# Performance work log

Hardware: AMD Instinct MI355X
Metric: run time of the kernel (lower is better)

The kernel has to match this reference:

```python
import jax, jax.numpy as jnp
import numpy as np

BN_EPS = 1e-5


def setup_inputs() -> dict:
    key = jax.random.key(0)
    ks = jax.random.split(key, 4)
    B, N, D = 8, 8192, 256
    outD = 256
    s = 1.0 / np.sqrt(D)
    return {
        "feature": jax.random.normal(ks[0], (B, N, D), dtype=jnp.float32),
        "W_qk": jax.random.normal(ks[1], (2, D, D), dtype=jnp.float32) * s,
        "b_qk": jnp.zeros((2, D), dtype=jnp.float32),
        "W_v": jax.random.normal(ks[2], (D, outD), dtype=jnp.float32) * s,
        "b_v": jnp.zeros((outD,), dtype=jnp.float32),
        "gamma": jnp.ones((D,), dtype=jnp.float32),
        "beta": jnp.zeros((D,), dtype=jnp.float32),
    }


def reference(feature, W_qk, b_qk, W_v, b_v, gamma, beta):
    # QK: [B, 2, N, D]
    QK = jnp.einsum("bnd,kde->bkne", feature, W_qk) + b_qk[None, :, None, :]
    # value: [B, N, outD]
    value = jnp.einsum("bnd,de->bne", feature, W_v) + b_v
    query = QK[:, 0]  # [B, N, D]
    key = QK[:, 1]    # [B, N, D]
    # softmax over the sequence axis (dim=1), per (batch, channel)
    sm = jax.nn.softmax(key, axis=1)
    # lambda context: softmax^T @ value -> [B, D, outD]
    lam = jnp.einsum("bnd,bne->bde", sm, value)
    # BatchNorm1d(featureDim) in training mode: channel axis = D (axis 1),
    # stats over (batch, spatial) = axes (0, 2); biased variance as torch uses.
    mean = jnp.mean(lam, axis=(0, 2), keepdims=True)
    var = jnp.var(lam, axis=(0, 2), keepdims=True)
    bn = (lam - mean) * jax.lax.rsqrt(var + BN_EPS)
    bn = bn * gamma[None, :, None] + beta[None, :, None]
    # result: query @ BN -> [B, N, outD]
    return jnp.einsum("bnd,bde->bne", query, bn)
```

## Files before the change

kernel.cpp:

```cpp
#include <hip/hip_runtime.h>

typedef unsigned short u16;
typedef __bf16 bf16x8 __attribute__((ext_vector_type(8)));
typedef float f32x4 __attribute__((ext_vector_type(4)));

#define LOG2E 1.44269504088896f

__device__ inline u16 f2b(float f) {
    unsigned u = __float_as_uint(f);
    u += 0x7fff + ((u >> 16) & 1);
    return (u16)(u >> 16);
}
__device__ inline float b2f(u16 u) { return __uint_as_float(((unsigned)u) << 16); }
__device__ inline unsigned pk2(float a, float b) {
    return (unsigned)f2b(a) | ((unsigned)f2b(b) << 16);
}
__device__ inline uint4 pack8(float4 a, float4 b) {
    return uint4{pk2(a.x, a.y), pk2(a.z, a.w), pk2(b.x, b.y), pk2(b.z, b.w)};
}
__device__ inline f32x4 mfma_bf16(uint4 a, uint4 b, f32x4 c) {
    return __builtin_amdgcn_mfma_f32_16x16x32_bf16(
        __builtin_bit_cast(bf16x8, a), __builtin_bit_cast(bf16x8, b), c, 0, 0, 0);
}
__device__ inline void ld16(const u16* g, u16* l) {
    __builtin_amdgcn_global_load_lds(
        (const __attribute__((address_space(1))) unsigned int*)g,
        (__attribute__((address_space(3))) unsigned int*)l, 16, 0, 0);
}
__device__ inline uint4 expfrag(uint4 v, float nc) {
    float e[8];
#pragma unroll
    for (int i = 0; i < 4; ++i) {
        unsigned u = ((const unsigned*)&v)[i];
        e[2 * i] = exp2f(fmaf(b2f((u16)(u & 0xffff)), LOG2E, nc));
        e[2 * i + 1] = exp2f(fmaf(b2f((u16)(u >> 16)), LOG2E, nc));
    }
    uint4 r;
    asm("v_cvt_pk_bf16_f32 %0, %1, %2" : "=v"(r.x) : "v"(e[0]), "v"(e[1]));
    asm("v_cvt_pk_bf16_f32 %0, %1, %2" : "=v"(r.y) : "v"(e[2]), "v"(e[3]));
    asm("v_cvt_pk_bf16_f32 %0, %1, %2" : "=v"(r.z) : "v"(e[4]), "v"(e[5]));
    asm("v_cvt_pk_bf16_f32 %0, %1, %2" : "=v"(r.w) : "v"(e[6]), "v"(e[7]));
    return r;
}


__global__ __launch_bounds__(256) void prep_w(const float* __restrict__ Wqk,
                                              const float* __restrict__ Wv,
                                              u16* __restrict__ WkT,
                                              u16* __restrict__ WvT,
                                              u16* __restrict__ Wqb) {
    int idx = blockIdx.x * 256 + threadIdx.x;
    int which = idx >> 16;
    int i = (idx >> 8) & 255;
    int j = idx & 255;
    if (which == 0)
        WkT[i * 256 + j] = f2b(Wqk[65536 + j * 256 + i]);
    else if (which == 1)
        WvT[i * 256 + j] = f2b(Wv[j * 256 + i]);
    else
        Wqb[i * 256 + j] = f2b(Wqk[i * 256 + j]);
}

__global__ __launch_bounds__(256, 2) void gemm_kv(const float* __restrict__ A,
                                                  const u16* __restrict__ BtK,
                                                  const u16* __restrict__ BtV,
                                                  const float* __restrict__ biasK,
                                                  const float* __restrict__ biasV,
                                                  u16* __restrict__ KT,
                                                  u16* __restrict__ VT,
                                                  float* __restrict__ partial) {
    __shared__ __align__(16) u16 lds[36864];

    const int t = threadIdx.x;
    const int r0 = blockIdx.x * 64;
    const int w = t >> 6, lane = t & 63, l15 = lane & 15, q = lane >> 4;
    const int sq = ((lane & 3) ^ ((lane >> 3) & 3)) * 8;
    const int qs = (q ^ ((l15 >> 1) & 3)) * 8;
    const int awoff = (t >> 2) * 32 + sq;
    const int brr = t >> 2;

    f32x4 accK[4][4], accV[4][4];
#pragma unroll
    for (int rt = 0; rt < 4; ++rt)
#pragma unroll
        for (int ct = 0; ct < 4; ++ct) {
            accK[rt][ct] = f32x4{0.f, 0.f, 0.f, 0.f};
            accV[rt][ct] = f32x4{0.f, 0.f, 0.f, 0.f};
        }

    const float* Arow = A + (long)(r0 + brr) * 256 + (t & 3) * 8;
    float4 p0 = ((const float4*)Arow)[0], p1 = ((const float4*)Arow)[1];
    float4 c0_ = *(const float4*)(Arow + 32), c1_ = *(const float4*)(Arow + 36);
    float4 d0_ = *(const float4*)(Arow + 64), d1_ = *(const float4*)(Arow + 68);

    {
        u16* dK = lds + 4096 + w * 512;
#pragma unroll
        for (int j = 0; j < 4; ++j) {
            int br = j * 64 + brr;
            ld16(BtK + br * 256 + sq, dK + j * 2048);
            ld16(BtV + br * 256 + sq, dK + 8192 + j * 2048);
        }
    }
    *(uint4*)(lds + awoff) = pack8(p0, p1);
    __syncthreads();

#pragma unroll
    for (int t8 = 0; t8 < 8; ++t8) {
        const int cur = t8 & 1;
        if (t8 < 7) {
            const int k0 = (t8 + 1) * 32;
            u16* dK = lds + 4096 + (cur ^ 1) * 16384 + w * 512;
#pragma unroll
            for (int j = 0; j < 4; ++j) {
                int br = j * 64 + brr;
                ld16(BtK + br * 256 + k0 + sq, dK + j * 2048);
                ld16(BtV + br * 256 + k0 + sq, dK + 8192 + j * 2048);
            }
            *(uint4*)(lds + (cur ^ 1) * 2048 + awoff) = pack8(c0_, c1_);
            c0_ = d0_; c1_ = d1_;
            if (t8 < 5) {
                d0_ = *(const float4*)(Arow + (t8 + 3) * 32);
                d1_ = *(const float4*)(Arow + (t8 + 3) * 32 + 4);
            }
        }
        const u16* Asc = lds + cur * 2048;
        const u16* Bc = lds + 4096 + cur * 16384;
        uint4 af[4];
#pragma unroll
        for (int rt = 0; rt < 4; ++rt)
            af[rt] = *(const uint4*)(Asc + (rt * 16 + l15) * 32 + qs);
#pragma unroll
        for (int ct = 0; ct < 4; ++ct) {
            const int bo = (w * 64 + ct * 16 + l15) * 32 + qs;
            uint4 bK = *(const uint4*)(Bc + bo);
            uint4 bV = *(const uint4*)(Bc + 8192 + bo);
#pragma unroll
            for (int rt = 0; rt < 4; ++rt) {
                accK[rt][ct] = mfma_bf16(af[rt], bK, accK[rt][ct]);
                accV[rt][ct] = mfma_bf16(af[rt], bV, accV[rt][ct]);
            }
        }
        __syncthreads();
    }

    const int bb = r0 >> 13;
    const int nt0 = (r0 & 8191) >> 5;
    const int nch = nt0 >> 1;
    u16* Ct = lds;
#pragma unroll
    for (int pass = 0; pass < 2; ++pass) {
        const f32x4(*acc)[4] = pass ? accV : accK;
        const float* bias = pass ? biasV : biasK;
        u16* CT = pass ? VT : KT;
#pragma unroll
        for (int ct = 0; ct < 4; ++ct) {
            const int col = w * 64 + ct * 16 + l15;
            const float bv = bias[col];
            ushort4 pks[4];
#pragma unroll
            for (int rt = 0; rt < 4; ++rt) {
                ushort4 pk;
                pk.x = f2b(acc[rt][ct][0] + bv);
                pk.y = f2b(acc[rt][ct][1] + bv);
                pk.z = f2b(acc[rt][ct][2] + bv);
                pk.w = f2b(acc[rt][ct][3] + bv);
                pks[rt] = pk;
                *(ushort4*)&Ct[col * 72 + rt * 16 + q * 4] = pk;
            }
            if (pass == 0) {
                float zm = -1e30f;
#pragma unroll
                for (int rt = 0; rt < 4; ++rt)
                    zm = fmaxf(zm,
                               fmaxf(fmaxf(b2f(pks[rt].x), b2f(pks[rt].y)),
                                     fmaxf(b2f(pks[rt].z), b2f(pks[rt].w))));
                zm = fmaxf(zm, __shfl_xor(zm, 16, 64));
                zm = fmaxf(zm, __shfl_xor(zm, 32, 64));
                zm *= LOG2E;
                float zs = 0.f;
#pragma unroll
                for (int rt = 0; rt < 4; ++rt) {
                    zs += exp2f(fmaf(b2f(pks[rt].x), LOG2E, -zm));
                    zs += exp2f(fmaf(b2f(pks[rt].y), LOG2E, -zm));
                    zs += exp2f(fmaf(b2f(pks[rt].z), LOG2E, -zm));
                    zs += exp2f(fmaf(b2f(pks[rt].w), LOG2E, -zm));
                }
                zs += __shfl_xor(zs, 16, 64);
                zs += __shfl_xor(zs, 32, 64);
                if (q == 0) {
                    float* pp =
                        partial + (((long)(bb * 128 + nch)) * 256 + col) * 2;
                    pp[0] = zm;
                    pp[1] = zs;
                }
            }
        }
        __syncthreads();
        {
            const long tb = (((long)(bb * 256 + nt0)) * 256 + t) * 32;
#pragma unroll
            for (int j2 = 0; j2 < 2; ++j2)
#pragma unroll
                for (int g = 0; g < 4; ++g)
                    *(uint4*)(CT + tb + j2 * 8192 + g * 8) =
                        *(const uint4*)&Ct[t * 72 + j2 * 32 + g * 8];
        }
        __syncthreads();
    }
}

__global__ __launch_bounds__(256) void stats2(const float* __restrict__ partial,
                                              float* __restrict__ ctab) {
    const int b = blockIdx.x, d = threadIdx.x;
    float M = -1e30f;
    for (int i = 0; i < 128; ++i)
        M = fmaxf(M, partial[(((long)(b * 128 + i)) * 256 + d) * 2]);
    float S = 0.f;
    for (int i = 0; i < 128; ++i) {
        const float* pp = partial + (((long)(b * 128 + i)) * 256 + d) * 2;
        S += pp[1] * exp2f(pp[0] - M);
    }
    ctab[b * 256 + d] = M + log2f(S);
}

__global__ __launch_bounds__(256, 3) void gemm_out(const float* __restrict__ A,
                                                   const u16* __restrict__ WfoldT,
                                                   const float* __restrict__ outb,
                                                   float* __restrict__ C) {
    __shared__ __align__(16) u16 lds[20480];
    const int t = threadIdx.x;
    const int r0 = blockIdx.x * 64;
    const int bb = r0 >> 13;
    const int w = t >> 6, lane = t & 63, l15 = lane & 15, q = lane >> 4;
    const int sq = ((lane & 3) ^ ((lane >> 3) & 3)) * 8;
    const int qs = (q ^ ((l15 >> 1) & 3)) * 8;
    const int awoff = (t >> 2) * 32 + sq;
    const int brr = t >> 2;
    const u16* Bt = WfoldT + (long)bb * 65536;

    f32x4 acc[4][4];
#pragma unroll
    for (int rt = 0; rt < 4; ++rt)
#pragma unroll
        for (int ct = 0; ct < 4; ++ct) acc[rt][ct] = f32x4{0.f, 0.f, 0.f, 0.f};

    const float* Arow = A + (long)(r0 + brr) * 256 + (t & 3) * 8;
    float4 p0 = ((const float4*)Arow)[0], p1 = ((const float4*)Arow)[1];
    float4 c0_ = *(const float4*)(Arow + 32), c1_ = *(const float4*)(Arow + 36);
    float4 d0_ = *(const float4*)(Arow + 64), d1_ = *(const float4*)(Arow + 68);

    {
        u16* dB = lds + 4096 + w * 512;
#pragma unroll
        for (int j = 0; j < 4; ++j)
            ld16(Bt + (j * 64 + brr) * 256 + sq, dB + j * 2048);
    }
    *(uint4*)(lds + awoff) = pack8(p0, p1);
    __syncthreads();

#pragma unroll
    for (int t8 = 0; t8 < 8; ++t8) {
        const int cur = t8 & 1;
        if (t8 < 7) {
            const int k0 = (t8 + 1) * 32;
            u16* dB = lds + 4096 + (cur ^ 1) * 8192 + w * 512;
#pragma unroll
            for (int j = 0; j < 4; ++j)
                ld16(Bt + (j * 64 + brr) * 256 + k0 + sq, dB + j * 2048);
            *(uint4*)(lds + (cur ^ 1) * 2048 + awoff) = pack8(c0_, c1_);
            c0_ = d0_; c1_ = d1_;
            if (t8 < 5) {
                d0_ = *(const float4*)(Arow + (t8 + 3) * 32);
                d1_ = *(const float4*)(Arow + (t8 + 3) * 32 + 4);
            }
        }
        const u16* Asc = lds + cur * 2048;
        const u16* Bc = lds + 4096 + cur * 8192;
        uint4 af[4];
#pragma unroll
        for (int rt = 0; rt < 4; ++rt)
            af[rt] = *(const uint4*)(Asc + (rt * 16 + l15) * 32 + qs);
#pragma unroll
        for (int ct = 0; ct < 4; ++ct) {
            uint4 bf = *(const uint4*)(Bc + (w * 64 + ct * 16 + l15) * 32 + qs);
#pragma unroll
            for (int rt = 0; rt < 4; ++rt)
                acc[rt][ct] = mfma_bf16(af[rt], bf, acc[rt][ct]);
        }
        __syncthreads();
    }

#pragma unroll
    for (int ct = 0; ct < 4; ++ct) {
        const int col = w * 64 + ct * 16 + l15;
        const float bv = outb[bb * 256 + col];
#pragma unroll
        for (int rt = 0; rt < 4; ++rt) {
            const long rbase = r0 + rt * 16 + q * 4;
#pragma unroll
            for (int r = 0; r < 4; ++r)
                C[(rbase + r) * 256 + col] = acc[rt][ct][r] + bv;
        }
    }
}

__global__ __launch_bounds__(256, 2) void gemm_splitk(const u16* __restrict__ VT,
                                                      const u16* __restrict__ KT,
                                                      const float* __restrict__ ctab,
                                                      float* __restrict__ lamP,
                                                      int chunk) {
    __shared__ __align__(16) u16 lds[16384];
    const int t = threadIdx.x;
    const int r0 = blockIdx.x * 128;
    const int c0 = blockIdx.y * 128;
    const int s = blockIdx.z;
    const int bA = r0 >> 8, e0 = r0 & 255;
    const int w = t >> 6, lane = t & 63, l15 = lane & 15, q = lane >> 4;
    const int sq = ((lane & 3) ^ ((lane >> 3) & 3)) * 8;
    const int qs = (q ^ ((l15 >> 1) & 3)) * 8;
    const int brr = t >> 2;

    const int nt_base = (int)(((long)s * chunk) >> 5);
    const u16* Abase = VT + (((long)bA * 256 + nt_base) * 256 + e0) * 32;
    const u16* Bbase = KT + (((long)bA * 256 + nt_base) * 256 + c0) * 32;

    const float nc0 = -ctab[bA * 256 + c0 + w * 32 + l15];
    const float nc1 = -ctab[bA * 256 + c0 + w * 32 + 16 + l15];

    f32x4 acc[8][2];
#pragma unroll
    for (int rt = 0; rt < 8; ++rt) {
        acc[rt][0] = f32x4{0.f, 0.f, 0.f, 0.f};
        acc[rt][1] = f32x4{0.f, 0.f, 0.f, 0.f};
    }

    {
        u16* dA = lds + w * 512;
#pragma unroll
        for (int j = 0; j < 2; ++j) {
            int br = j * 64 + brr;
            ld16(Abase + br * 32 + sq, dA + j * 2048);
            ld16(Bbase + br * 32 + sq, dA + 4096 + j * 2048);
        }
    }
    __syncthreads();

    const int nk = chunk >> 5;
    for (int ks = 0; ks < nk; ++ks) {
        const int cur = ks & 1;
        if (ks + 1 < nk) {
            const long toff = (long)(ks + 1) * 8192;
            u16* dA = lds + (cur ^ 1) * 8192 + w * 512;
#pragma unroll
            for (int j = 0; j < 2; ++j) {
                int br = j * 64 + brr;
                ld16(Abase + toff + br * 32 + sq, dA + j * 2048);
                ld16(Bbase + toff + br * 32 + sq, dA + 4096 + j * 2048);
            }
        }
        const u16* Asc = lds + cur * 8192;
        const u16* Bsc = Asc + 4096;
        const int bo = (w * 32 + l15) * 32 + qs;
        uint4 bf0 = expfrag(*(const uint4*)(Bsc + bo), nc0);
        uint4 bf1 = expfrag(*(const uint4*)(Bsc + 512 + bo), nc1);
#pragma unroll
        for (int rt = 0; rt < 8; ++rt) {
            uint4 af = *(const uint4*)(Asc + (rt * 16 + l15) * 32 + qs);
            acc[rt][0] = mfma_bf16(af, bf0, acc[rt][0]);
            acc[rt][1] = mfma_bf16(af, bf1, acc[rt][1]);
        }
        __syncthreads();
    }

    float* outp = lamP + (long)s * 524288;
#pragma unroll
    for (int rt = 0; rt < 8; ++rt)
#pragma unroll
        for (int ct = 0; ct < 2; ++ct) {
            const int col = c0 + w * 32 + ct * 16 + l15;
#pragma unroll
            for (int r = 0; r < 4; ++r)
                outp[(long)(r0 + rt * 16 + q * 4 + r) * 256 + col] =
                    acc[rt][ct][r];
        }
}

__global__ __launch_bounds__(256) void reduce_lam(const float* __restrict__ lamP,
                                                  float* __restrict__ lamT, int S) {
    int i = blockIdx.x * 256 + threadIdx.x;
    float4 v = ((const float4*)lamP)[i];
    for (int s = 1; s < S; ++s) {
        float4 p = ((const float4*)(lamP + (long)s * 524288))[i];
        v.x += p.x; v.y += p.y; v.z += p.z; v.w += p.w;
    }
    ((float4*)lamT)[i] = v;
}

__global__ __launch_bounds__(256, 4) void gemm_fold(const u16* __restrict__ Abn,
                                                    const u16* __restrict__ Wqb,
                                                    u16* __restrict__ WfoldT) {
    __shared__ __align__(16) u16 lds[4096];
    u16* As = lds;
    u16* Bs = lds + 2048;

    const int t = threadIdx.x;
    const int r0 = blockIdx.x * 64;
    const int c0 = blockIdx.y * 64;
    const int w = t >> 6, lane = t & 63, l15 = lane & 15, q = lane >> 4;

    f32x4 acc[4];
#pragma unroll
    for (int c = 0; c < 4; ++c) acc[c] = f32x4{0.f, 0.f, 0.f, 0.f};

    const int br = t >> 2;
    const int bk = (t & 3) * 8;

    for (int k0 = 0; k0 < 256; k0 += 32) {
        ld16(Abn + (long)(r0 + br) * 256 + k0 + bk, As + w * 512);
        ld16(Wqb + (long)(c0 + br) * 256 + k0 + bk, Bs + w * 512);
        __syncthreads();
        uint4 af = *(const uint4*)(As + (w * 16 + l15) * 32 + q * 8);
#pragma unroll
        for (int c = 0; c < 4; ++c) {
            uint4 bf = *(const uint4*)(Bs + (c * 16 + l15) * 32 + q * 8);
            acc[c] = mfma_bf16(af, bf, acc[c]);
        }
        __syncthreads();
    }

#pragma unroll
    for (int c = 0; c < 4; ++c) {
        int col = c0 + c * 16 + l15;
#pragma unroll
        for (int r = 0; r < 4; ++r) {
            int row = r0 + w * 16 + q * 4 + r;
            WfoldT[(long)row * 256 + col] = f2b(acc[c][r]);
        }
    }
}

__global__ __launch_bounds__(256) void bn_kernel(const float* __restrict__ lamT,
                                                 const float* __restrict__ gamma,
                                                 const float* __restrict__ beta,
                                                 u16* __restrict__ bnT) {
    const int d = blockIdx.x;
    const int t = threadIdx.x;
    float vals[8];
    float s = 0.f, ss = 0.f;
#pragma unroll
    for (int i = 0; i < 8; ++i) {
        float v = lamT[(long)(i * 256 + t) * 256 + d];
        vals[i] = v;
        s += v;
        ss += v * v;
    }
#pragma unroll
    for (int sh = 32; sh > 0; sh >>= 1) {
        s += __shfl_xor(s, sh, 64);
        ss += __shfl_xor(ss, sh, 64);
    }
    __shared__ float red[8];
    int w = t >> 6;
    if ((t & 63) == 0) {
        red[w] = s;
        red[w + 4] = ss;
    }
    __syncthreads();
    s = red[0] + red[1] + red[2] + red[3];
    ss = red[4] + red[5] + red[6] + red[7];
    float mean = s * (1.f / 2048.f);
    float var = ss * (1.f / 2048.f) - mean * mean;
    float scale = gamma[d] * rsqrtf(var + 1e-5f);
    float shift = beta[d] - mean * scale;
#pragma unroll
    for (int i = 0; i < 8; ++i)
        bnT[(long)(i * 256 + t) * 256 + d] = f2b(vals[i] * scale + shift);
}

__global__ __launch_bounds__(256) void outb_kernel(const float* __restrict__ bq,
                                                   const u16* __restrict__ bnT,
                                                   float* __restrict__ outb) {
    int b = blockIdx.x, e = threadIdx.x;
    const u16* rowp = bnT + ((long)b * 256 + e) * 256;
    float s = 0.f;
    for (int dd = 0; dd < 256; ++dd) s += bq[dd] * b2f(rowp[dd]);
    outb[b * 256 + e] = s;
}

extern "C" void kernel_launch(void* const* d_in, const int* in_sizes, int n_in,
                              void* d_out, int out_size, void* d_ws, size_t ws_size,
                              hipStream_t stream) {
    const float* feat = (const float*)d_in[0];
    const float* W_qk = (const float*)d_in[1];
    const float* b_qk = (const float*)d_in[2];
    const float* W_v = (const float*)d_in[3];
    const float* b_v = (const float*)d_in[4];
    const float* gamma = (const float*)d_in[5];
    const float* beta = (const float*)d_in[6];
    float* out = (float*)d_out;

    char* ws = (char*)d_ws;
    u16* KT = (u16*)(ws);
    u16* VT = (u16*)(ws + 33554432);
    u16* WkT = (u16*)(ws + 67108864);
    u16* WvT = (u16*)(ws + 67239936);
    u16* Wqb = (u16*)(ws + 67371008);
    float* partial = (float*)(ws + 67502080);
    float* ctab = (float*)(ws + 69599232);
    const size_t base = 69607424;
    float* lamP = (float*)(ws + base);
    size_t avail = (ws_size > base) ? ws_size - base : 0;
    int S = (avail >= 16u * 2097152u) ? 16
          : (avail >= 8u * 2097152u) ? 8
          : (avail >= 4u * 2097152u) ? 4 : 2;
    float* lamT = (float*)ws;
    u16* bnT = (u16*)(ws + 2097152);
    u16* WfoldT = (u16*)(ws + 3145728);
    float* outb = (float*)(ws + 4194304);

    prep_w<<<768, 256, 0, stream>>>(W_qk, W_v, WkT, WvT, Wqb);
    gemm_kv<<<1024, 256, 0, stream>>>(feat, WkT, WvT, b_qk + 256, b_v, KT, VT,
                                      partial);
    stats2<<<8, 256, 0, stream>>>(partial, ctab);
    gemm_splitk<<<dim3(16, 2, S), 256, 0, stream>>>(VT, KT, ctab, lamP, 8192 / S);
    reduce_lam<<<512, 256, 0, stream>>>(lamP, lamT, S);
    bn_kernel<<<256, 256, 0, stream>>>(lamT, gamma, beta, bnT);
    outb_kernel<<<8, 256, 0, stream>>>(b_qk, bnT, outb);
    gemm_fold<<<dim3(32, 4), 256, 0, stream>>>(bnT, Wqb, WfoldT);
    gemm_out<<<1024, 256, 0, stream>>>(feat, WfoldT, outb, out);
}
```

Measured before the change: 272.8 us.

## Widen split-K lambda GEMM tiles and parallelize softmax stats reduction

The split-K lambda GEMM now has one 512-thread block per (batch, split) compute the full 256x256 output. Each K tile is loaded once and shared across all output columns, where before a 128x128 tiling loaded each V and K slab several times. The exp fragment work on K is likewise no longer repeated across row blocks. Separately, stats2 now uses 64 blocks with an online max/sum merge through shared memory, replacing 8 blocks of serial loops. The trade-off is far fewer blocks in the lambda GEMM (8*S, 128 at S=16), which may underfill the GPU, plus more registers per thread.

```diff
diff --git a/kernel.cpp b/kernel.cpp
--- a/kernel.cpp
+++ b/kernel.cpp
@@ -212,16 +212,34 @@
 
 __global__ __launch_bounds__(256) void stats2(const float* __restrict__ partial,
                                               float* __restrict__ ctab) {
-    const int b = blockIdx.x, d = threadIdx.x;
-    float M = -1e30f;
-    for (int i = 0; i < 128; ++i)
-        M = fmaxf(M, partial[(((long)(b * 128 + i)) * 256 + d) * 2]);
-    float S = 0.f;
-    for (int i = 0; i < 128; ++i) {
+    const int b = blockIdx.x, dg = blockIdx.y;
+    const int t = threadIdx.x;
+    const int d = dg * 32 + (t & 31);
+    const int ci = t >> 5;
+    float m = -1e30f, sum = 0.f;
+#pragma unroll 4
+    for (int k = 0; k < 16; ++k) {
+        int i = ci * 16 + k;
         const float* pp = partial + (((long)(b * 128 + i)) * 256 + d) * 2;
-        S += pp[1] * exp2f(pp[0] - M);
-    }
-    ctab[b * 256 + d] = M + log2f(S);
+        float mi = pp[0], si = pp[1];
+        float M = fmaxf(m, mi);
+        sum = sum * exp2f(m - M) + si * exp2f(mi - M);
+        m = M;
+    }
+    __shared__ float red[512];
+    red[t] = m;
+    red[t + 256] = sum;
+    __syncthreads();
+    if (ci == 0) {
+#pragma unroll
+        for (int j = 1; j < 8; ++j) {
+            float mi = red[t + j * 32], si = red[t + 256 + j * 32];
+            float M = fmaxf(m, mi);
+            sum = sum * exp2f(m - M) + si * exp2f(mi - M);
+            m = M;
+        }
+        ctab[b * 256 + d] = m + log2f(sum);
+    }
 }
 
 __global__ __launch_bounds__(256, 3) void gemm_out(const float* __restrict__ A,
@@ -305,84 +323,85 @@
     }
 }
 
-__global__ __launch_bounds__(256, 2) void gemm_splitk(const u16* __restrict__ VT,
-                                                      const u16* __restrict__ KT,
-                                                      const float* __restrict__ ctab,
-                                                      float* __restrict__ lamP,
-                                                      int chunk) {
-    __shared__ __align__(16) u16 lds[16384];
+__global__ __launch_bounds__(512, 2) void gemm_lam(const u16* __restrict__ VT,
+                                                   const u16* __restrict__ KT,
+                                                   const float* __restrict__ ctab,
+                                                   float* __restrict__ lamP,
+                                                   int nk) {
+    __shared__ __align__(16) u16 lds[32768];
     const int t = threadIdx.x;
-    const int r0 = blockIdx.x * 128;
-    const int c0 = blockIdx.y * 128;
-    const int s = blockIdx.z;
-    const int bA = r0 >> 8, e0 = r0 & 255;
+    const int b = blockIdx.x;
+    const int s = blockIdx.y;
     const int w = t >> 6, lane = t & 63, l15 = lane & 15, q = lane >> 4;
+    const int eg = w >> 2, dg = w & 3;
     const int sq = ((lane & 3) ^ ((lane >> 3) & 3)) * 8;
     const int qs = (q ^ ((l15 >> 1) & 3)) * 8;
-    const int brr = t >> 2;
-
-    const int nt_base = (int)(((long)s * chunk) >> 5);
-    const u16* Abase = VT + (((long)bA * 256 + nt_base) * 256 + e0) * 32;
-    const u16* Bbase = KT + (((long)bA * 256 + nt_base) * 256 + c0) * 32;
-
-    const float nc0 = -ctab[bA * 256 + c0 + w * 32 + l15];
-    const float nc1 = -ctab[bA * 256 + c0 + w * 32 + 16 + l15];
-
-    f32x4 acc[8][2];
-#pragma unroll
-    for (int rt = 0; rt < 8; ++rt) {
-        acc[rt][0] = f32x4{0.f, 0.f, 0.f, 0.f};
-        acc[rt][1] = f32x4{0.f, 0.f, 0.f, 0.f};
-    }
-
-    {
-        u16* dA = lds + w * 512;
-#pragma unroll
-        for (int j = 0; j < 2; ++j) {
-            int br = j * 64 + brr;
-            ld16(Abase + br * 32 + sq, dA + j * 2048);
-            ld16(Bbase + br * 32 + sq, dA + 4096 + j * 2048);
-        }
-    }
+
+    const int nt0 = s * nk;
+    const u16* Vb = VT + ((long)(b * 256 + nt0)) * 8192;
+    const u16* Kb = KT + ((long)(b * 256 + nt0)) * 8192;
+
+    float nc[4];
+#pragma unroll
+    for (int ct = 0; ct < 4; ++ct)
+        nc[ct] = -ctab[b * 256 + dg * 64 + ct * 16 + l15];
+
+    f32x4 acc[8][4];
+#pragma unroll
+    for (int rt = 0; rt < 8; ++rt)
+#pragma unroll
+        for (int ct = 0; ct < 4; ++ct) acc[rt][ct] = f32x4{0.f, 0.f, 0.f, 0.f};
+
+#define STAGE_TILE(tile, buf)                                                  \
+    {                                                                          \
+        _Pragma("unroll") for (int j = 0; j < 2; ++j) {                        \
+            int g = j * 512 + t;                                               \
+            ld16((tile) + (g >> 2) * 32 + sq, (buf) + (j * 512 + w * 64) * 8); \
+        }                                                                      \
+    }
+
+    STAGE_TILE(Vb, lds)
+    STAGE_TILE(Kb, lds + 8192)
     __syncthreads();
 
-    const int nk = chunk >> 5;
     for (int ks = 0; ks < nk; ++ks) {
         const int cur = ks & 1;
         if (ks + 1 < nk) {
-            const long toff = (long)(ks + 1) * 8192;
-            u16* dA = lds + (cur ^ 1) * 8192 + w * 512;
-#pragma unroll
-            for (int j = 0; j < 2; ++j) {
-                int br = j * 64 + brr;
-                ld16(Abase + toff + br * 32 + sq, dA + j * 2048);
-                ld16(Bbase + toff + br * 32 + sq, dA + 4096 + j * 2048);
-            }
-        }
-        const u16* Asc = lds + cur * 8192;
-        const u16* Bsc = Asc + 4096;
-        const int bo = (w * 32 + l15) * 32 + qs;
-        uint4 bf0 = expfrag(*(const uint4*)(Bsc + bo), nc0);
-        uint4 bf1 = expfrag(*(const uint4*)(Bsc + 512 + bo), nc1);
+            const u16* Vn = Vb + (long)(ks + 1) * 8192;
+            const u16* Kn = Kb + (long)(ks + 1) * 8192;
+            u16* dst = lds + (cur ^ 1) * 16384;
+            STAGE_TILE(Vn, dst)
+            STAGE_TILE(Kn, dst + 8192)
+        }
+        const u16* Vs = lds + cur * 16384;
+        const u16* Ks = Vs + 8192;
+        uint4 bf[4];
+#pragma unroll
+        for (int ct = 0; ct < 4; ++ct)
+            bf[ct] = expfrag(
+                *(const uint4*)(Ks + (dg * 64 + ct * 16 + l15) * 32 + qs),
+                nc[ct]);
 #pragma unroll
         for (int rt = 0; rt < 8; ++rt) {
-            uint4 af = *(const uint4*)(Asc + (rt * 16 + l15) * 32 + qs);
-            acc[rt][0] = mfma_bf16(af, bf0, acc[rt][0]);
-            acc[rt][1] = mfma_bf16(af, bf1, acc[rt][1]);
-        }
-        __syncthreads();
-    }
-
-    float* outp = lamP + (long)s * 524288;
+            uint4 af = *(const uint4*)(Vs + (eg * 128 + rt * 16 + l15) * 32 + qs);
+#pragma unroll
+            for (int ct = 0; ct < 4; ++ct)
+                acc[rt][ct] = mfma_bf16(af, bf[ct], acc[rt][ct]);
+        }
+        __syncthreads();
+    }
+#undef STAGE_TILE
+
+    float* outp = lamP + (long)s * 524288 + (long)b * 65536;
 #pragma unroll
     for (int rt = 0; rt < 8; ++rt)
 #pragma unroll
-        for (int ct = 0; ct < 2; ++ct) {
-            const int col = c0 + w * 32 + ct * 16 + l15;
+        for (int ct = 0; ct < 4; ++ct) {
+            const int col = dg * 64 + ct * 16 + l15;
+            const int row = eg * 128 + rt * 16 + q * 4;
 #pragma unroll
             for (int r = 0; r < 4; ++r)
-                outp[(long)(r0 + rt * 16 + q * 4 + r) * 256 + col] =
-                    acc[rt][ct][r];
+                outp[(long)(row + r) * 256 + col] = acc[rt][ct][r];
         }
 }
 
@@ -522,8 +541,8 @@
     prep_w<<<768, 256, 0, stream>>>(W_qk, W_v, WkT, WvT, Wqb);
     gemm_kv<<<1024, 256, 0, stream>>>(feat, WkT, WvT, b_qk + 256, b_v, KT, VT,
                                       partial);
-    stats2<<<8, 256, 0, stream>>>(partial, ctab);
-    gemm_splitk<<<dim3(16, 2, S), 256, 0, stream>>>(VT, KT, ctab, lamP, 8192 / S);
+    stats2<<<dim3(8, 8), 256, 0, stream>>>(partial, ctab);
+    gemm_lam<<<dim3(8, S), 512, 0, stream>>>(VT, KT, ctab, lamP, 8192 / S / 32);
     reduce_lam<<<512, 256, 0, stream>>>(lamP, lamT, S);
     bn_kernel<<<256, 256, 0, stream>>>(lamT, gamma, beta, bnT);
     outb_kernel<<<8, 256, 0, stream>>>(b_qk, bnT, outb);
```

Result: faster. 261.1 us (-4.3%).
